# Optimization experiments

Measured on AMD Instinct MI355X. Metric: run time of the kernel, lower is better.

## Reference

```python
import jax, jax.numpy as jnp
import numpy as np

B, R, M, L, H = 256, 2048, 65536, 64, 4  # batch, reservoir, memory_size, key_len, read_heads


def setup_inputs() -> dict:
    key = jax.random.key(0)
    ks = jax.random.split(key, 4)
    s = 1.0 / np.sqrt(R).astype(np.float32)  # ~xavier scale for Linear weights
    return {
        "reservoir_state": jax.random.normal(ks[0], (B, R), dtype=jnp.float32),
        "memory": jax.random.normal(ks[1], (1, M, L), dtype=jnp.float32),
        "Wk": jax.random.normal(ks[2], (H * L, R), dtype=jnp.float32) * s,
        "bk": jnp.zeros((H * L,), dtype=jnp.float32),
        "Wb": jax.random.normal(ks[3], (H, R), dtype=jnp.float32) * s,
        "bb": jnp.zeros((H,), dtype=jnp.float32),
    }


def reference(reservoir_state, memory, Wk, bk, Wb, bb):
    b = reservoir_state.shape[0]
    h = Wb.shape[0]
    # key projection -> [B, H, L]
    keys = (reservoir_state @ Wk.T + bk).reshape(b, h, -1)
    # per-head key strength, relu-gated -> [B, H]
    betas = jax.nn.relu(reservoir_state @ Wb.T + bb)
    # content addressing: dot(keys, memory rows) -> [B, H, M]
    dots = jnp.einsum('bhl,ml->bhm', keys, memory[0])
    # normalize by key norm (as in original: sqrt(sum(keys^2)))
    dots = dots / jnp.sqrt(jnp.sum(keys ** 2, axis=-1, keepdims=True))
    # beta-scaled softmax over memory slots
    return jax.nn.softmax(betas[:, :, None] * dots, axis=-1)
```

## Files before the change

### kernel.cpp

```cpp
#include <hip/hip_runtime.h>
#include <hip/hip_bf16.h>

#define BB   256
#define RR   2048
#define MM   65536
#define LL   64
#define HH   4
#define NROW 1024
#define KEYS 256

typedef float f32x4 __attribute__((ext_vector_type(4)));
typedef short short8 __attribute__((ext_vector_type(8)));

#define MFMA(A,B,C) __builtin_amdgcn_mfma_f32_16x16x32_bf16((A),(B),(C),0,0,0)

__device__ __forceinline__ unsigned short bf16_rn(float x) {
    union { float f; unsigned int u; } v; v.f = x;
    unsigned int r = v.u + 0x7FFFu + ((v.u >> 16) & 1u);
    return (unsigned short)(r >> 16);
}
__device__ __forceinline__ float bf16_to_f(unsigned short h) {
    union { float f; unsigned int u; } v; v.u = ((unsigned int)h) << 16; return v.f;
}
__device__ __forceinline__ void split8_store(const float* x, unsigned short* hi, unsigned short* lo) {
    unsigned int ph[4], pl[4];
#pragma unroll
    for (int j = 0; j < 4; ++j) {
        unsigned short h0 = bf16_rn(x[2*j]),   l0 = bf16_rn(x[2*j]   - bf16_to_f(h0));
        unsigned short h1 = bf16_rn(x[2*j+1]), l1 = bf16_rn(x[2*j+1] - bf16_to_f(h1));
        ph[j] = (unsigned int)h0 | ((unsigned int)h1 << 16);
        pl[j] = (unsigned int)l0 | ((unsigned int)l1 << 16);
    }
    ((uint4*)hi)[0] = make_uint4(ph[0], ph[1], ph[2], ph[3]);
    ((uint4*)lo)[0] = make_uint4(pl[0], pl[1], pl[2], pl[3]);
}

__global__ __launch_bounds__(256) void transpose_k(const float* __restrict__ in,
                                                   float* __restrict__ out,
                                                   int NR, int NC) {
    __shared__ float t[64 * 65];
    int r0 = blockIdx.x * 64, c0 = blockIdx.y * 64;
    int lane = threadIdx.x & 63, w = threadIdx.x >> 6;
#pragma unroll
    for (int i = 0; i < 16; ++i) {
        int rr = i * 4 + w;
        t[lane * 65 + rr] = in[(size_t)(r0 + rr) * NC + c0 + lane];
    }
    __syncthreads();
#pragma unroll
    for (int i = 0; i < 16; ++i) {
        int cc = i * 4 + w;
        out[(size_t)(c0 + cc) * NR + r0 + lane] = t[cc * 65 + lane];
    }
}

__global__ __launch_bounds__(256) void normmax_k(const float* __restrict__ mem,
                                                 float* __restrict__ normpart) {
    int row = blockIdx.x * 256 + threadIdx.x;
    const float4* p = (const float4*)(mem + (size_t)row * LL);
    float s = 0.f;
#pragma unroll
    for (int i = 0; i < 16; ++i) { float4 v = p[i]; s += v.x*v.x + v.y*v.y + v.z*v.z + v.w*v.w; }
    int lane = threadIdx.x & 63, w = threadIdx.x >> 6;
#pragma unroll
    for (int off = 1; off < 64; off <<= 1) s = fmaxf(s, __shfl_xor(s, off, 64));
    __shared__ float sm[4];
    if (lane == 0) sm[w] = s;
    __syncthreads();
    if (threadIdx.x == 0)
        normpart[blockIdx.x] = fmaxf(fmaxf(sm[0], sm[1]), fmaxf(sm[2], sm[3]));
}

__global__ __launch_bounds__(256) void prep_mem(const float* __restrict__ mem,
                                                unsigned short* __restrict__ bhi,
                                                unsigned short* __restrict__ blo) {
    int gid = blockIdx.x * 256 + threadIdx.x;
    int lane = gid & 63, frag = gid >> 6;
    int t = frag >> 1, c = frag & 1;
    int mrow = t * 16 + (lane & 15);
    int k0 = c * 32 + (lane >> 4) * 8;
    const float4* src = (const float4*)(mem + (size_t)mrow * LL + k0);
    float4 x0 = src[0], x1 = src[1];
    float x[8] = {x0.x, x0.y, x0.z, x0.w, x1.x, x1.y, x1.z, x1.w};
    split8_store(x, bhi + (size_t)gid * 8, blo + (size_t)gid * 8);
}

__global__ __launch_bounds__(256) void k0_keys(const float* __restrict__ S,
                                               const float* __restrict__ WkT,
                                               float* __restrict__ kpart) {
    __shared__ float sl[8 * 256];
    int bg = blockIdx.x, kc = blockIdx.y, tid = threadIdx.x;
    int b0 = bg * 8;
#pragma unroll
    for (int bi = 0; bi < 8; ++bi)
        sl[bi * 256 + tid] = S[(size_t)(b0 + bi) * RR + kc * 256 + tid];
    __syncthreads();
    float acc[8] = {0,0,0,0,0,0,0,0};
    const float* wp = WkT + (size_t)kc * 256 * KEYS + tid;
#pragma unroll 4
    for (int kk = 0; kk < 256; ++kk) {
        float wv = wp[kk * KEYS];
#pragma unroll
        for (int bi = 0; bi < 8; ++bi)
            acc[bi] = fmaf(sl[bi * 256 + kk], wv, acc[bi]);
    }
    float* op = kpart + (size_t)kc * BB * KEYS + (size_t)b0 * KEYS + tid;
#pragma unroll
    for (int bi = 0; bi < 8; ++bi)
        op[bi * KEYS] = acc[bi];
}

__global__ __launch_bounds__(256) void k1_finalize(const float* __restrict__ S,
                                                   const float* __restrict__ kpart,
                                                   const float* __restrict__ bk,
                                                   const float* __restrict__ Wb,
                                                   const float* __restrict__ bb,
                                                   const float* __restrict__ normpart,
                                                   float* __restrict__ q_rm,
                                                   float* __restrict__ brow) {
    int bh = blockIdx.x, b = bh >> 2, h = bh & 3;
    int tid = threadIdx.x, lane = tid & 63, w = tid >> 6;
    float p = 0.f;
#pragma unroll
    for (int i = 0; i < 8; ++i) {
        int k = i * 256 + tid;
        p += S[(size_t)b * RR + k] * Wb[(size_t)h * RR + k];
    }
    float nm = normpart[tid];
#pragma unroll
    for (int off = 1; off < 64; off <<= 1) {
        p  += __shfl_xor(p, off, 64);
        nm  = fmaxf(nm, __shfl_xor(nm, off, 64));
    }
    __shared__ float red[4], redm[4];
    if (lane == 0) { red[w] = p; redm[w] = nm; }
    __syncthreads();
    if (tid < 64) {
        float beta = red[0] + red[1] + red[2] + red[3] + bb[h];
        beta = fmaxf(beta, 0.f);
        float maxn = sqrtf(fmaxf(fmaxf(redm[0], redm[1]), fmaxf(redm[2], redm[3])));
        float kv = bk[h * LL + lane];
#pragma unroll
        for (int c = 0; c < 8; ++c)
            kv += kpart[(size_t)c * BB * KEYS + (size_t)b * KEYS + h * LL + lane];
        float sq = kv * kv;
#pragma unroll
        for (int off = 1; off < 64; off <<= 1) sq += __shfl_xor(sq, off, 64);
        float scale = beta / sqrtf(sq);
        q_rm[(size_t)bh * LL + lane] = kv * scale;
        if (lane == 0) brow[bh] = beta * maxn;
    }
}

__global__ __launch_bounds__(256) void prep_a(const float* __restrict__ q_rm,
                                              unsigned short* __restrict__ ahi,
                                              unsigned short* __restrict__ alo) {
    int gid = blockIdx.x * 256 + threadIdx.x;
    int lane = gid & 63, frag = gid >> 6;
    int rtg = frag >> 1, c = frag & 1;
    int row = rtg * 16 + (lane & 15);
    int k0 = c * 32 + (lane >> 4) * 8;
    const float4* src = (const float4*)(q_rm + (size_t)row * LL + k0);
    float4 x0 = src[0], x1 = src[1];
    float x[8] = {x0.x, x0.y, x0.z, x0.w, x1.x, x1.y, x1.z, x1.w};
    split8_store(x, ahi + (size_t)gid * 8, alo + (size_t)gid * 8);
}

__global__ __launch_bounds__(256) void k2_mfma(const unsigned short* __restrict__ bhi,
                                               const unsigned short* __restrict__ blo,
                                               const unsigned short* __restrict__ ahi,
                                               const unsigned short* __restrict__ alo,
                                               const float* __restrict__ brow,
                                               float* __restrict__ psum) {
    int bx = blockIdx.x;
    int mblk = bx >> 4, rg = bx & 15;
    int tid = threadIdx.x, w = tid >> 6, lane = tid & 63;
    int g = lane >> 4;
    short8 Ah[4][2], Al[4][2];
#pragma unroll
    for (int rt = 0; rt < 4; ++rt)
#pragma unroll
        for (int c = 0; c < 2; ++c) {
            size_t off = ((size_t)((rg * 4 + rt) * 2 + c) * 64 + lane) * 8;
            Ah[rt][c] = *(const short8*)(ahi + off);
            Al[rt][c] = *(const short8*)(alo + off);
        }
    float br[4][4];
#pragma unroll
    for (int rt = 0; rt < 4; ++rt)
#pragma unroll
        for (int r = 0; r < 4; ++r)
            br[rt][r] = brow[rg * 64 + rt * 16 + g * 4 + r];
    float s[4][4] = {{0.f}};
    int t0 = mblk * 64 + w * 16;
    for (int ti = 0; ti < 16; ++ti) {
        int t = t0 + ti;
        size_t o0 = ((size_t)(t * 2 + 0) * 64 + lane) * 8;
        size_t o1 = ((size_t)(t * 2 + 1) * 64 + lane) * 8;
        short8 Bh0 = *(const short8*)(bhi + o0);
        short8 Bh1 = *(const short8*)(bhi + o1);
        short8 Bl0 = *(const short8*)(blo + o0);
        short8 Bl1 = *(const short8*)(blo + o1);
#pragma unroll
        for (int rt = 0; rt < 4; ++rt) {
            f32x4 C = {0.f, 0.f, 0.f, 0.f};
            C = MFMA(Ah[rt][0], Bh0, C);
            C = MFMA(Ah[rt][1], Bh1, C);
            C = MFMA(Al[rt][0], Bh0, C);
            C = MFMA(Al[rt][1], Bh1, C);
            C = MFMA(Ah[rt][0], Bl0, C);
            C = MFMA(Ah[rt][1], Bl1, C);
#pragma unroll
            for (int r = 0; r < 4; ++r)
                s[rt][r] += __expf(C[r] - br[rt][r]);
        }
    }
#pragma unroll
    for (int rt = 0; rt < 4; ++rt)
#pragma unroll
        for (int r = 0; r < 4; ++r) {
            float v = s[rt][r];
            v += __shfl_xor(v, 1, 64);
            v += __shfl_xor(v, 2, 64);
            v += __shfl_xor(v, 4, 64);
            v += __shfl_xor(v, 8, 64);
            s[rt][r] = v;
        }
    if ((lane & 15) == 0) {
        int col = mblk * 4 + w;
#pragma unroll
        for (int rt = 0; rt < 4; ++rt)
#pragma unroll
            for (int r = 0; r < 4; ++r) {
                int row = rg * 64 + rt * 16 + g * 4 + r;
                psum[(size_t)row * 256 + col] = s[rt][r];
            }
    }
}

__global__ __launch_bounds__(256) void k3_combine(const float* __restrict__ psum,
                                                  float* __restrict__ ginv) {
    int row = blockIdx.x, tid = threadIdx.x, lane = tid & 63, w = tid >> 6;
    float v = psum[(size_t)row * 256 + tid];
#pragma unroll
    for (int off = 1; off < 64; off <<= 1) v += __shfl_xor(v, off, 64);
    __shared__ float sm[4];
    if (lane == 0) sm[w] = v;
    __syncthreads();
    if (tid == 0) ginv[row] = 1.0f / (sm[0] + sm[1] + sm[2] + sm[3]);
}

__global__ __launch_bounds__(256) void k4_mfma(const unsigned short* __restrict__ bhi,
                                               const unsigned short* __restrict__ blo,
                                               const unsigned short* __restrict__ ahi,
                                               const unsigned short* __restrict__ alo,
                                               const float* __restrict__ brow,
                                               const float* __restrict__ ginv,
                                               float* __restrict__ out) {
    int bx = blockIdx.x;
    int mblk = bx >> 4, rg = bx & 15;
    int tid = threadIdx.x, w = tid >> 6, lane = tid & 63;
    int g = lane >> 4;
    short8 Ah[4][2], Al[4][2];
#pragma unroll
    for (int rt = 0; rt < 4; ++rt)
#pragma unroll
        for (int c = 0; c < 2; ++c) {
            size_t off = ((size_t)((rg * 4 + rt) * 2 + c) * 64 + lane) * 8;
            Ah[rt][c] = *(const short8*)(ahi + off);
            Al[rt][c] = *(const short8*)(alo + off);
        }
    float br[4][4], gv[4][4];
    size_t rbase[4][4];
#pragma unroll
    for (int rt = 0; rt < 4; ++rt)
#pragma unroll
        for (int r = 0; r < 4; ++r) {
            int row = rg * 64 + rt * 16 + g * 4 + r;
            br[rt][r] = brow[row];
            gv[rt][r] = ginv[row];
            rbase[rt][r] = (size_t)row * MM + (lane & 15);
        }
    int t0 = mblk * 64 + w * 16;
    for (int ti = 0; ti < 16; ++ti) {
        int t = t0 + ti;
        size_t o0 = ((size_t)(t * 2 + 0) * 64 + lane) * 8;
        size_t o1 = ((size_t)(t * 2 + 1) * 64 + lane) * 8;
        short8 Bh0 = *(const short8*)(bhi + o0);
        short8 Bh1 = *(const short8*)(bhi + o1);
        short8 Bl0 = *(const short8*)(blo + o0);
        short8 Bl1 = *(const short8*)(blo + o1);
#pragma unroll
        for (int rt = 0; rt < 4; ++rt) {
            f32x4 C = {0.f, 0.f, 0.f, 0.f};
            C = MFMA(Ah[rt][0], Bh0, C);
            C = MFMA(Ah[rt][1], Bh1, C);
            C = MFMA(Al[rt][0], Bh0, C);
            C = MFMA(Al[rt][1], Bh1, C);
            C = MFMA(Ah[rt][0], Bl0, C);
            C = MFMA(Ah[rt][1], Bl1, C);
#pragma unroll
            for (int r = 0; r < 4; ++r) {
                float o = __expf(C[r] - br[rt][r]) * gv[rt][r];
                __builtin_nontemporal_store(o, out + rbase[rt][r] + (size_t)t * 16);
            }
        }
    }
}

extern "C" void kernel_launch(void* const* d_in, const int* in_sizes, int n_in,
                              void* d_out, int out_size, void* d_ws, size_t ws_size,
                              hipStream_t stream) {
    const float* S   = (const float*)d_in[0];
    const float* mem = (const float*)d_in[1];
    const float* Wk  = (const float*)d_in[2];
    const float* bk  = (const float*)d_in[3];
    const float* Wb  = (const float*)d_in[4];
    const float* bb  = (const float*)d_in[5];
    float* out = (float*)d_out;

    float* WkT      = (float*)d_ws;
    float* kpart    = WkT   + (size_t)RR * KEYS;
    float* q_rm     = kpart + (size_t)8 * BB * KEYS;
    float* psum     = q_rm  + (size_t)NROW * LL;
    float* brow     = psum  + (size_t)NROW * 256;
    float* ginv     = brow  + NROW;
    float* normpart = ginv  + NROW;
    unsigned short* bhi = (unsigned short*)(normpart + 256);
    unsigned short* blo = bhi + (size_t)8192 * 512;
    unsigned short* ahi = blo + (size_t)8192 * 512;
    unsigned short* alo = ahi + (size_t)128 * 512;

    transpose_k<<<dim3(BB / 64, RR / 64), 256, 0, stream>>>(Wk, WkT, KEYS, RR);
    normmax_k  <<<256,         256, 0, stream>>>(mem, normpart);
    prep_mem   <<<2048,        256, 0, stream>>>(mem, bhi, blo);
    k0_keys    <<<dim3(32, 8), 256, 0, stream>>>(S, WkT, kpart);
    k1_finalize<<<NROW,        256, 0, stream>>>(S, kpart, bk, Wb, bb, normpart, q_rm, brow);
    prep_a     <<<32,          256, 0, stream>>>(q_rm, ahi, alo);
    k2_mfma    <<<1024,        256, 0, stream>>>(bhi, blo, ahi, alo, brow, psum);
    k3_combine <<<NROW,        256, 0, stream>>>(psum, ginv);
    k4_mfma    <<<1024,        256, 0, stream>>>(bhi, blo, ahi, alo, brow, ginv, out);
}
```

Before: 397.1 us.

## Fuse memory prep, norm max and Wk transpose; add XCD-aware block mapping

Merges the Wk transpose, the memory row-norm max and the bf16 hi/lo split of memory into one kernel. The norm is computed from values already loaded for the split, which removes a second full read of memory and two launches. The k2/k4 MFMA kernels get an XCD-aware block index decode so blocks on the same XCD share memory tiles in L2, plus unroll-2 on the main loop. The trade-off is that normpart grows to 2048 partials, which k1 now reduces, and the unroll may raise register pressure.

```diff
diff --git a/kernel.cpp b/kernel.cpp
--- a/kernel.cpp
+++ b/kernel.cpp
@@ -35,54 +35,57 @@
     ((uint4*)lo)[0] = make_uint4(pl[0], pl[1], pl[2], pl[3]);
 }
 
-__global__ __launch_bounds__(256) void transpose_k(const float* __restrict__ in,
-                                                   float* __restrict__ out,
-                                                   int NR, int NC) {
-    __shared__ float t[64 * 65];
-    int r0 = blockIdx.x * 64, c0 = blockIdx.y * 64;
-    int lane = threadIdx.x & 63, w = threadIdx.x >> 6;
-#pragma unroll
-    for (int i = 0; i < 16; ++i) {
-        int rr = i * 4 + w;
-        t[lane * 65 + rr] = in[(size_t)(r0 + rr) * NC + c0 + lane];
-    }
-    __syncthreads();
-#pragma unroll
-    for (int i = 0; i < 16; ++i) {
-        int cc = i * 4 + w;
-        out[(size_t)(c0 + cc) * NR + r0 + lane] = t[cc * 65 + lane];
-    }
-}
-
-__global__ __launch_bounds__(256) void normmax_k(const float* __restrict__ mem,
-                                                 float* __restrict__ normpart) {
-    int row = blockIdx.x * 256 + threadIdx.x;
-    const float4* p = (const float4*)(mem + (size_t)row * LL);
-    float s = 0.f;
-#pragma unroll
-    for (int i = 0; i < 16; ++i) { float4 v = p[i]; s += v.x*v.x + v.y*v.y + v.z*v.z + v.w*v.w; }
-    int lane = threadIdx.x & 63, w = threadIdx.x >> 6;
-#pragma unroll
-    for (int off = 1; off < 64; off <<= 1) s = fmaxf(s, __shfl_xor(s, off, 64));
-    __shared__ float sm[4];
-    if (lane == 0) sm[w] = s;
-    __syncthreads();
-    if (threadIdx.x == 0)
-        normpart[blockIdx.x] = fmaxf(fmaxf(sm[0], sm[1]), fmaxf(sm[2], sm[3]));
-}
-
-__global__ __launch_bounds__(256) void prep_mem(const float* __restrict__ mem,
-                                                unsigned short* __restrict__ bhi,
-                                                unsigned short* __restrict__ blo) {
-    int gid = blockIdx.x * 256 + threadIdx.x;
-    int lane = gid & 63, frag = gid >> 6;
-    int t = frag >> 1, c = frag & 1;
-    int mrow = t * 16 + (lane & 15);
-    int k0 = c * 32 + (lane >> 4) * 8;
-    const float4* src = (const float4*)(mem + (size_t)mrow * LL + k0);
-    float4 x0 = src[0], x1 = src[1];
-    float x[8] = {x0.x, x0.y, x0.z, x0.w, x1.x, x1.y, x1.z, x1.w};
-    split8_store(x, bhi + (size_t)gid * 8, blo + (size_t)gid * 8);
+__global__ __launch_bounds__(256) void prep_fused(const float* __restrict__ mem,
+                                                  const float* __restrict__ Wk,
+                                                  unsigned short* __restrict__ bhi,
+                                                  unsigned short* __restrict__ blo,
+                                                  float* __restrict__ normpart,
+                                                  float* __restrict__ WkT) {
+    int blk = blockIdx.x;
+    int tid = threadIdx.x;
+    if (blk < 2048) {
+        __shared__ float cs[64];
+        int gid = blk * 256 + tid;
+        int lane = gid & 63, frag = gid >> 6;
+        int t = frag >> 1, c = frag & 1;
+        int mrow = t * 16 + (lane & 15);
+        int k0 = c * 32 + (lane >> 4) * 8;
+        const float4* src = (const float4*)(mem + (size_t)mrow * LL + k0);
+        float4 x0 = src[0], x1 = src[1];
+        float x[8] = {x0.x, x0.y, x0.z, x0.w, x1.x, x1.y, x1.z, x1.w};
+        split8_store(x, bhi + (size_t)gid * 8, blo + (size_t)gid * 8);
+        float sq = 0.f;
+#pragma unroll
+        for (int j = 0; j < 8; ++j) sq += x[j] * x[j];
+        sq += __shfl_xor(sq, 16, 64);
+        sq += __shfl_xor(sq, 32, 64);
+        int w = tid >> 6;
+        if (lane < 16) cs[w * 16 + lane] = sq;
+        __syncthreads();
+        if (tid < 32) {
+            int tt = tid >> 4, rr = tid & 15;
+            float s = cs[(tt * 2) * 16 + rr] + cs[(tt * 2 + 1) * 16 + rr];
+#pragma unroll
+            for (int off = 1; off < 32; off <<= 1) s = fmaxf(s, __shfl_xor(s, off, 64));
+            if (tid == 0) normpart[blk] = s;
+        }
+    } else {
+        __shared__ float tbuf[64 * 65];
+        int tx = blk - 2048;
+        int r0 = (tx & 3) * 64, c0 = (tx >> 2) * 64;
+        int lane = tid & 63, w = tid >> 6;
+#pragma unroll
+        for (int i = 0; i < 16; ++i) {
+            int rr = i * 4 + w;
+            tbuf[lane * 65 + rr] = Wk[(size_t)(r0 + rr) * RR + c0 + lane];
+        }
+        __syncthreads();
+#pragma unroll
+        for (int i = 0; i < 16; ++i) {
+            int cc = i * 4 + w;
+            WkT[(size_t)(c0 + cc) * KEYS + r0 + lane] = tbuf[cc * 65 + lane];
+        }
+    }
 }
 
 __global__ __launch_bounds__(256) void k0_keys(const float* __restrict__ S,
@@ -126,7 +129,9 @@
         int k = i * 256 + tid;
         p += S[(size_t)b * RR + k] * Wb[(size_t)h * RR + k];
     }
-    float nm = normpart[tid];
+    float nm = 0.f;
+#pragma unroll
+    for (int i = 0; i < 8; ++i) nm = fmaxf(nm, normpart[i * 256 + tid]);
 #pragma unroll
     for (int off = 1; off < 64; off <<= 1) {
         p  += __shfl_xor(p, off, 64);
@@ -166,14 +171,20 @@
     split8_store(x, ahi + (size_t)gid * 8, alo + (size_t)gid * 8);
 }
 
+__device__ __forceinline__ void decode_bx(int bx, int& mblk, int& rg) {
+    int xcd = bx & 7;
+    int tmp = bx >> 3;
+    rg = tmp & 15;
+    mblk = (tmp >> 4) * 8 + xcd;
+}
+
 __global__ __launch_bounds__(256) void k2_mfma(const unsigned short* __restrict__ bhi,
                                                const unsigned short* __restrict__ blo,
                                                const unsigned short* __restrict__ ahi,
                                                const unsigned short* __restrict__ alo,
                                                const float* __restrict__ brow,
                                                float* __restrict__ psum) {
-    int bx = blockIdx.x;
-    int mblk = bx >> 4, rg = bx & 15;
+    int mblk, rg; decode_bx(blockIdx.x, mblk, rg);
     int tid = threadIdx.x, w = tid >> 6, lane = tid & 63;
     int g = lane >> 4;
     short8 Ah[4][2], Al[4][2];
@@ -193,6 +204,7 @@
             br[rt][r] = brow[rg * 64 + rt * 16 + g * 4 + r];
     float s[4][4] = {{0.f}};
     int t0 = mblk * 64 + w * 16;
+#pragma unroll 2
     for (int ti = 0; ti < 16; ++ti) {
         int t = t0 + ti;
         size_t o0 = ((size_t)(t * 2 + 0) * 64 + lane) * 8;
@@ -257,8 +269,7 @@
                                                const float* __restrict__ brow,
                                                const float* __restrict__ ginv,
                                                float* __restrict__ out) {
-    int bx = blockIdx.x;
-    int mblk = bx >> 4, rg = bx & 15;
+    int mblk, rg; decode_bx(blockIdx.x, mblk, rg);
     int tid = threadIdx.x, w = tid >> 6, lane = tid & 63;
     int g = lane >> 4;
     short8 Ah[4][2], Al[4][2];
@@ -282,6 +293,7 @@
             rbase[rt][r] = (size_t)row * MM + (lane & 15);
         }
     int t0 = mblk * 64 + w * 16;
+#pragma unroll 2
     for (int ti = 0; ti < 16; ++ti) {
         int t = t0 + ti;
         size_t o0 = ((size_t)(t * 2 + 0) * 64 + lane) * 8;
@@ -326,14 +338,12 @@
     float* brow     = psum  + (size_t)NROW * 256;
     float* ginv     = brow  + NROW;
     float* normpart = ginv  + NROW;
-    unsigned short* bhi = (unsigned short*)(normpart + 256);
+    unsigned short* bhi = (unsigned short*)(normpart + 2048);
     unsigned short* blo = bhi + (size_t)8192 * 512;
     unsigned short* ahi = blo + (size_t)8192 * 512;
     unsigned short* alo = ahi + (size_t)128 * 512;
 
-    transpose_k<<<dim3(BB / 64, RR / 64), 256, 0, stream>>>(Wk, WkT, KEYS, RR);
-    normmax_k  <<<256,         256, 0, stream>>>(mem, normpart);
-    prep_mem   <<<2048,        256, 0, stream>>>(mem, bhi, blo);
+    prep_fused <<<2176,        256, 0, stream>>>(mem, Wk, bhi, blo, normpart, WkT);
     k0_keys    <<<dim3(32, 8), 256, 0, stream>>>(S, WkT, kpart);
     k1_finalize<<<NROW,        256, 0, stream>>>(S, kpart, bk, Wb, bb, normpart, q_rm, brow);
     prep_a     <<<32,          256, 0, stream>>>(q_rm, ahi, alo);
```

After: 408.5 us. 1.03x slower.
